# Performance work log

Hardware: AMD Instinct MI355X
Metric: run time of the kernel (lower is better)

Reference implementation:

```python
import jax, jax.numpy as jnp
import numpy as np

N, P, Q, T, J, B, H = 262144, 64, 64, 2048, 512, 8, 64


def setup_inputs() -> dict:
    key = jax.random.key(0)
    ks = jax.random.split(key, 11)
    sH = 1.0 / np.sqrt(H).astype(np.float32)
    return {
        "idx": jax.random.randint(ks[0], (B,), 0, J),
        "seg_ids": jnp.sort(jax.random.randint(ks[1], (N,), 0, T)),
        "K": jax.random.normal(ks[2], (N, P), jnp.float32) * 0.1,
        "V": jax.random.normal(ks[3], (N, Q), jnp.float32),
        "S": jax.random.normal(ks[4], (P, J), jnp.float32) * 0.1,
        "W_ih": jax.random.normal(ks[5], (3 * H, Q), jnp.float32) * sH,
        "W_hh": jax.random.normal(ks[6], (3 * H, H), jnp.float32) * sH,
        "b_ih": jax.random.normal(ks[7], (3 * H,), jnp.float32) * sH,
        "b_hh": jax.random.normal(ks[8], (3 * H,), jnp.float32) * sH,
        "w_out": jax.random.normal(ks[9], (1, H), jnp.float32) * sH,
        "b_out": jax.random.normal(ks[10], (1,), jnp.float32) * sH,
    }


def reference(idx, seg_ids, K, V, S, W_ih, W_hh, b_ih, b_hh, w_out, b_out):
    # W[:, b] = K @ S[:, idx[b]]  -> [N, B]
    w = K @ S[:, idx]
    # ragged per-segment softmax over the N axis (segments = date windows)
    m = jax.ops.segment_max(w, seg_ids, num_segments=T)          # [T, B]
    e = jnp.exp(w - m[seg_ids])                                  # [N, B]
    denom = jax.ops.segment_sum(e, seg_ids, num_segments=T)     # [T, B]
    alpha = e / denom[seg_ids]                                   # [N, B]
    # weighted aggregation of V rows per segment: M[t, b] = sum_u alpha_u * V_u
    M = jax.ops.segment_sum(alpha[:, :, None] * V[:, None, :],
                            seg_ids, num_segments=T)             # [T, B, Q]
    X = jnp.transpose(M, (1, 0, 2))                              # [B, T, Q]

    # PyTorch GRU (gate order r,z,n). Faithful to the original bug: GRU was
    # built without batch_first=True, so axis 0 (B) is time, axis 1 (T) is batch.
    def step(h, x_t):  # x_t: [T, Q], h: [T, H]
        gi = x_t @ W_ih.T + b_ih                                 # [T, 3H]
        gh = h @ W_hh.T + b_hh                                   # [T, 3H]
        i_r, i_z, i_n = jnp.split(gi, 3, axis=1)
        h_r, h_z, h_n = jnp.split(gh, 3, axis=1)
        r = jax.nn.sigmoid(i_r + h_r)
        z = jax.nn.sigmoid(i_z + h_z)
        n = jnp.tanh(i_n + r * h_n)
        h_new = (1.0 - z) * n + z * h
        return h_new, h_new

    h0 = jnp.zeros((T, H), X.dtype)
    _, hs = jax.lax.scan(step, h0, X)                            # [B, T, H]
    preds = hs @ w_out.T + b_out                                 # [B, T, 1]
    return preds
```

## Files before the change

### kernel.cpp

```cpp
#include <hip/hip_runtime.h>
#include <math.h>

#define NN 262144
#define PP 64
#define QQ 64
#define TT 2048
#define JJ 512
#define BB 8
#define HH 64

__device__ __forceinline__ float lane_bcast(float v, int l) {
  return __int_as_float(__builtin_amdgcn_readlane(__float_as_int(v), l));
}

__global__ void k_prep(const int* __restrict__ seg_ids, const int* __restrict__ idx,
                       const float* __restrict__ S, int* __restrict__ seg_start,
                       float* __restrict__ s_cols) {
  int tid = blockIdx.x * blockDim.x + threadIdx.x;
  if (tid <= TT) {
    int lo = 0, hi = NN;
    while (lo < hi) {
      int mid = (lo + hi) >> 1;
      int v = seg_ids[mid];
      if (v < tid) lo = mid + 1; else hi = mid;
    }
    seg_start[tid] = lo;
  }
  int t2 = tid - (TT + 1);
  if (t2 >= 0 && t2 < PP * BB) {
    int p = t2 >> 3, b = t2 & 7;
    s_cols[b * PP + p] = S[p * JJ + idx[b]];
  }
}

__global__ __launch_bounds__(256) void k_w(const float* __restrict__ Kmat,
                                           const float* __restrict__ s_cols,
                                           float* __restrict__ ew) {
  __shared__ __align__(16) float s_lds[BB * PP];
  int tid = threadIdx.x;
  for (int i = tid; i < BB * PP; i += 256) s_lds[i] = s_cols[i];
  __syncthreads();
  int n = blockIdx.x * 64 + (tid >> 2);
  int sub = tid & 3;
  const float4* Kp = reinterpret_cast<const float4*>(Kmat + (size_t)n * PP + sub * 16);
  float4 kq[4];
#pragma unroll
  for (int j = 0; j < 4; ++j) kq[j] = Kp[j];
  float acc[8];
#pragma unroll
  for (int b = 0; b < 8; ++b) acc[b] = 0.f;
#pragma unroll
  for (int j4 = 0; j4 < 4; ++j4) {
    float4 kk = kq[j4];
#pragma unroll
    for (int b = 0; b < 8; ++b) {
      const float4 sv = *reinterpret_cast<const float4*>(&s_lds[b * PP + sub * 16 + j4 * 4]);
      acc[b] += kk.x * sv.x + kk.y * sv.y + kk.z * sv.z + kk.w * sv.w;
    }
  }
#pragma unroll
  for (int b = 0; b < 8; ++b) {
    acc[b] += __shfl_xor(acc[b], 1);
    acc[b] += __shfl_xor(acc[b], 2);
  }
  float ox = (sub == 0) ? acc[0] : (sub == 1) ? acc[2] : (sub == 2) ? acc[4] : acc[6];
  float oy = (sub == 0) ? acc[1] : (sub == 1) ? acc[3] : (sub == 2) ? acc[5] : acc[7];
  reinterpret_cast<float2*>(ew + (size_t)n * 8)[sub] =
      make_float2(__expf(ox), __expf(oy));
}

#define PSTRIDE 520
__global__ __launch_bounds__(256) void k_segp(const float* __restrict__ ew,
                                              const float* __restrict__ V,
                                              const int* __restrict__ seg_start,
                                              float* __restrict__ P) {
  int lane = threadIdx.x & 63, j = threadIdx.x >> 6;
  int t = blockIdx.x;
  int s = seg_start[t], e = seg_start[t + 1];
  int len = e - s;
  int chunk = (len + 3) >> 2;
  int b0 = s + j * chunk;
  int b1 = b0 + chunk; if (b1 > e) b1 = e;
  int slen = (b1 > b0) ? (b1 - b0) : 0;
  int rsub = lane >> 4;
  int qg = lane & 15;

  float4 acc[8];
#pragma unroll
  for (int b = 0; b < 8; ++b) acc[b] = make_float4(0.f, 0.f, 0.f, 0.f);
  float4 selo = make_float4(0.f, 0.f, 0.f, 0.f);
  float4 sehi = make_float4(0.f, 0.f, 0.f, 0.f);

#define PROC(RR)                                                                                           \
  {                                                                                                        \
    int r_ = (RR);                                                                                         \
    const float4* ewp_ = reinterpret_cast<const float4*>(ew + (size_t)r_ * 8);                             \
    float4 elo = ewp_[0], ehi = ewp_[1];                                                                   \
    float4 vv = reinterpret_cast<const float4*>(V + (size_t)r_ * QQ)[qg];                                  \
    selo.x += elo.x; selo.y += elo.y; selo.z += elo.z; selo.w += elo.w;                                    \
    sehi.x += ehi.x; sehi.y += ehi.y; sehi.z += ehi.z; sehi.w += ehi.w;                                    \
    acc[0].x += elo.x * vv.x; acc[0].y += elo.x * vv.y; acc[0].z += elo.x * vv.z; acc[0].w += elo.x * vv.w; \
    acc[1].x += elo.y * vv.x; acc[1].y += elo.y * vv.y; acc[1].z += elo.y * vv.z; acc[1].w += elo.y * vv.w; \
    acc[2].x += elo.z * vv.x; acc[2].y += elo.z * vv.y; acc[2].z += elo.z * vv.z; acc[2].w += elo.z * vv.w; \
    acc[3].x += elo.w * vv.x; acc[3].y += elo.w * vv.y; acc[3].z += elo.w * vv.z; acc[3].w += elo.w * vv.w; \
    acc[4].x += ehi.x * vv.x; acc[4].y += ehi.x * vv.y; acc[4].z += ehi.x * vv.z; acc[4].w += ehi.x * vv.w; \
    acc[5].x += ehi.y * vv.x; acc[5].y += ehi.y * vv.y; acc[5].z += ehi.y * vv.z; acc[5].w += ehi.y * vv.w; \
    acc[6].x += ehi.z * vv.x; acc[6].y += ehi.z * vv.y; acc[6].z += ehi.z * vv.z; acc[6].w += ehi.z * vv.w; \
    acc[7].x += ehi.w * vv.x; acc[7].y += ehi.w * vv.y; acc[7].z += ehi.w * vv.z; acc[7].w += ehi.w * vv.w; \
  }

  int nfull = slen >> 2, tail = slen & 3;
  for (int i = 0; i < nfull; ++i) PROC(b0 + i * 4 + rsub);
  if (tail && rsub < tail) PROC(b0 + nfull * 4 + rsub);
#undef PROC

#pragma unroll
  for (int b = 0; b < 8; ++b) {
    acc[b].x += __shfl_xor(acc[b].x, 16); acc[b].y += __shfl_xor(acc[b].y, 16);
    acc[b].z += __shfl_xor(acc[b].z, 16); acc[b].w += __shfl_xor(acc[b].w, 16);
    acc[b].x += __shfl_xor(acc[b].x, 32); acc[b].y += __shfl_xor(acc[b].y, 32);
    acc[b].z += __shfl_xor(acc[b].z, 32); acc[b].w += __shfl_xor(acc[b].w, 32);
  }
  selo.x += __shfl_xor(selo.x, 16); selo.y += __shfl_xor(selo.y, 16);
  selo.z += __shfl_xor(selo.z, 16); selo.w += __shfl_xor(selo.w, 16);
  sehi.x += __shfl_xor(sehi.x, 16); sehi.y += __shfl_xor(sehi.y, 16);
  sehi.z += __shfl_xor(sehi.z, 16); sehi.w += __shfl_xor(sehi.w, 16);
  selo.x += __shfl_xor(selo.x, 32); selo.y += __shfl_xor(selo.y, 32);
  selo.z += __shfl_xor(selo.z, 32); selo.w += __shfl_xor(selo.w, 32);
  sehi.x += __shfl_xor(sehi.x, 32); sehi.y += __shfl_xor(sehi.y, 32);
  sehi.z += __shfl_xor(sehi.z, 32); sehi.w += __shfl_xor(sehi.w, 32);

  float* Pp = P + ((size_t)t * 4 + j) * PSTRIDE;
  if (rsub == 0) {
#pragma unroll
    for (int b = 0; b < 8; ++b)
      *reinterpret_cast<float4*>(Pp + b * 64 + qg * 4) = acc[b];
    if (qg == 0) {
      Pp[512] = selo.x; Pp[513] = selo.y; Pp[514] = selo.z; Pp[515] = selo.w;
      Pp[516] = sehi.x; Pp[517] = sehi.y; Pp[518] = sehi.z; Pp[519] = sehi.w;
    }
  }
}

__global__ __launch_bounds__(256) void k_red(const float* __restrict__ P,
                                             float* __restrict__ M) {
  __shared__ float se[32];
  int t = blockIdx.x, tid = threadIdx.x;
  if (tid < 32) se[tid] = P[((size_t)t * 4 + (tid >> 3)) * PSTRIDE + 512 + (tid & 7)];
  __syncthreads();
  int o = tid * 2;
  int b = o >> 6;
  float dd = se[b] + se[8 + b] + se[16 + b] + se[24 + b];
  float inv = (dd > 0.f) ? 1.f / dd : 0.f;
  float sx = 0.f, sy = 0.f;
#pragma unroll
  for (int j = 0; j < 4; ++j) {
    float2 p = *reinterpret_cast<const float2*>(P + ((size_t)t * 4 + j) * PSTRIDE + o);
    sx += p.x; sy += p.y;
  }
  *reinterpret_cast<float2*>(M + (size_t)t * 512 + o) = make_float2(sx * inv, sy * inv);
}

__global__ __launch_bounds__(256) void k_gi(const float* __restrict__ M,
                                            const float* __restrict__ W_ih,
                                            const float* __restrict__ b_ih,
                                            float* __restrict__ GI) {
  __shared__ float Wt[64 * 193];
  int tid = threadIdx.x;
  for (int i = tid; i < 192 * 64; i += 256) {
    int g = i >> 6, k = i & 63;
    Wt[k * 193 + g] = W_ih[i];
  }
  __syncthreads();
  int lane = tid & 63, wv = tid >> 6;
  int row0 = blockIdx.x * 32 + wv * 8;
  float x[8];
#pragma unroll
  for (int rr = 0; rr < 8; ++rr) {
    int rho = row0 + rr;
    int b = rho >> 11, t = rho & 2047;
    x[rr] = M[((size_t)t * 8 + b) * 64 + lane];
  }
  float bi0 = b_ih[lane], bi1 = b_ih[64 + lane], bi2 = b_ih[128 + lane];
  float a0[8], a1[8], a2[8];
#pragma unroll
  for (int rr = 0; rr < 8; ++rr) { a0[rr] = bi0; a1[rr] = bi1; a2[rr] = bi2; }
#pragma unroll
  for (int k = 0; k < 64; ++k) {
    float w0 = Wt[k * 193 + lane];
    float w1 = Wt[k * 193 + 64 + lane];
    float w2 = Wt[k * 193 + 128 + lane];
#pragma unroll
    for (int rr = 0; rr < 8; ++rr) {
      float xk = lane_bcast(x[rr], k);
      a0[rr] += w0 * xk; a1[rr] += w1 * xk; a2[rr] += w2 * xk;
    }
  }
#pragma unroll
  for (int rr = 0; rr < 8; ++rr) {
    size_t rho = (size_t)row0 + rr;
    GI[rho * 192 + lane]       = a0[rr];
    GI[rho * 192 + 64 + lane]  = a1[rr];
    GI[rho * 192 + 128 + lane] = a2[rr];
  }
}

__global__ __launch_bounds__(256) void k_gru(const float* __restrict__ GI,
                                             const float* __restrict__ W_hh,
                                             const float* __restrict__ b_hh,
                                             const float* __restrict__ w_out,
                                             const float* __restrict__ b_out,
                                             float* __restrict__ preds) {
  __shared__ float Wt[64 * 193];
  int tid = threadIdx.x;
  for (int i = tid; i < 192 * 64; i += 256) {
    int g = i >> 6, k = i & 63;
    Wt[k * 193 + g] = W_hh[i];
  }
  __syncthreads();
  int lane = tid & 63, wv = tid >> 6;
  int t = blockIdx.x * 4 + wv;
  float bh0 = b_hh[lane], bh1 = b_hh[64 + lane], bh2 = b_hh[128 + lane];
  float wo = w_out[lane];
  float bo = b_out[0];

  float gr[8], gz[8], gn[8];
#pragma unroll
  for (int b = 0; b < 8; ++b) {
    size_t base = ((size_t)b * TT + t) * 192;
    gr[b] = GI[base + lane];
    gz[b] = GI[base + 64 + lane];
    gn[b] = GI[base + 128 + lane];
  }

  float h;
  {
    float r = 1.f / (1.f + __expf(-(gr[0] + bh0)));
    float z = 1.f / (1.f + __expf(-(gz[0] + bh1)));
    float nv = tanhf(gn[0] + r * bh2);
    h = (1.f - z) * nv;
    float pv = h * wo;
#pragma unroll
    for (int off = 32; off; off >>= 1) pv += __shfl_xor(pv, off);
    if (lane == 0) preds[t] = pv + bo;
  }
#pragma unroll
  for (int b = 1; b < 8; ++b) {
    float ar = bh0, az = bh1, an = bh2;
#pragma unroll
    for (int k = 0; k < 64; ++k) {
      float hk = lane_bcast(h, k);
      float w0 = Wt[k * 193 + lane];
      float w1 = Wt[k * 193 + 64 + lane];
      float w2 = Wt[k * 193 + 128 + lane];
      ar += w0 * hk; az += w1 * hk; an += w2 * hk;
    }
    float r = 1.f / (1.f + __expf(-(gr[b] + ar)));
    float z = 1.f / (1.f + __expf(-(gz[b] + az)));
    float nv = tanhf(gn[b] + r * an);
    h = (1.f - z) * nv + z * h;
    float pv = h * wo;
#pragma unroll
    for (int off = 32; off; off >>= 1) pv += __shfl_xor(pv, off);
    if (lane == 0) preds[(size_t)b * TT + t] = pv + bo;
  }
}

extern "C" void kernel_launch(void* const* d_in, const int* in_sizes, int n_in,
                              void* d_out, int out_size, void* d_ws, size_t ws_size,
                              hipStream_t stream) {
  const int*   idx     = (const int*)d_in[0];
  const int*   seg_ids = (const int*)d_in[1];
  const float* Kmat    = (const float*)d_in[2];
  const float* V       = (const float*)d_in[3];
  const float* S       = (const float*)d_in[4];
  const float* W_ih    = (const float*)d_in[5];
  const float* W_hh    = (const float*)d_in[6];
  const float* b_ih    = (const float*)d_in[7];
  const float* b_hh    = (const float*)d_in[8];
  const float* w_out   = (const float*)d_in[9];
  const float* b_out   = (const float*)d_in[10];
  float* out = (float*)d_out;

  char* ws = (char*)d_ws;
  int*   seg_start = (int*)(ws + 0);
  float* s_cols    = (float*)(ws + 8448);
  float* ew        = (float*)(ws + 10496);
  float* M         = (float*)(ws + 8399104);
  float* GI        = (float*)(ws + 12593408);
  float* P         = (float*)(ws + 25176320);

  hipLaunchKernelGGL(k_prep, dim3(11), dim3(256), 0, stream, seg_ids, idx, S, seg_start, s_cols);
  hipLaunchKernelGGL(k_w, dim3(NN / 64), dim3(256), 0, stream, Kmat, s_cols, ew);
  hipLaunchKernelGGL(k_segp, dim3(TT), dim3(256), 0, stream, ew, V, seg_start, P);
  hipLaunchKernelGGL(k_red, dim3(TT), dim3(256), 0, stream, P, M);
  hipLaunchKernelGGL(k_gi, dim3(512), dim3(256), 0, stream, M, W_ih, b_ih, GI);
  hipLaunchKernelGGL(k_gru, dim3(512), dim3(256), 0, stream, GI, W_hh, b_hh, w_out, b_out, out);
}
```

Baseline: 81.51 us.

## Process two GRU sequences per wave with swizzled float4 W_hh in LDS

The GRU kernel now keeps W_hh in row-major LDS with an XOR swizzle and reads it as float4, replacing the padded transposed scalar layout. Each wave advances two independent batch rows (t0, t0+1) so every weight load from LDS feeds two hidden states, and the grid shrinks from 512 to 256 blocks. The aim is to halve LDS traffic per step and increase ILP. The cost is higher register pressure and fewer blocks for the GPU's compute units.

```diff
diff --git a/kernel.cpp b/kernel.cpp
--- a/kernel.cpp
+++ b/kernel.cpp
@@ -211,58 +211,84 @@
                                              const float* __restrict__ w_out,
                                              const float* __restrict__ b_out,
                                              float* __restrict__ preds) {
-  __shared__ float Wt[64 * 193];
+  __shared__ __align__(16) float Wl[192 * 64];
   int tid = threadIdx.x;
-  for (int i = tid; i < 192 * 64; i += 256) {
-    int g = i >> 6, k = i & 63;
-    Wt[k * 193 + g] = W_hh[i];
+  for (int i = tid; i < 192 * 16; i += 256) {
+    int g = i >> 4, c = i & 15;
+    *reinterpret_cast<float4*>(&Wl[g * 64 + ((c ^ (g & 15)) * 4)]) =
+        *reinterpret_cast<const float4*>(W_hh + g * 64 + c * 4);
   }
   __syncthreads();
   int lane = tid & 63, wv = tid >> 6;
-  int t = blockIdx.x * 4 + wv;
+  int t0 = blockIdx.x * 8 + wv * 2;
   float bh0 = b_hh[lane], bh1 = b_hh[64 + lane], bh2 = b_hh[128 + lane];
   float wo = w_out[lane];
   float bo = b_out[0];
 
-  float gr[8], gz[8], gn[8];
+  float gr0[8], gz0[8], gn0[8], gr1[8], gz1[8], gn1[8];
 #pragma unroll
   for (int b = 0; b < 8; ++b) {
-    size_t base = ((size_t)b * TT + t) * 192;
-    gr[b] = GI[base + lane];
-    gz[b] = GI[base + 64 + lane];
-    gn[b] = GI[base + 128 + lane];
-  }
-
-  float h;
+    size_t base0 = ((size_t)b * TT + t0) * 192;
+    gr0[b] = GI[base0 + lane];
+    gz0[b] = GI[base0 + 64 + lane];
+    gn0[b] = GI[base0 + 128 + lane];
+    size_t base1 = base0 + 192;
+    gr1[b] = GI[base1 + lane];
+    gz1[b] = GI[base1 + 64 + lane];
+    gn1[b] = GI[base1 + 128 + lane];
+  }
+
+  const int sw = (lane & 15);
+  float h0, h1;
   {
-    float r = 1.f / (1.f + __expf(-(gr[0] + bh0)));
-    float z = 1.f / (1.f + __expf(-(gz[0] + bh1)));
-    float nv = tanhf(gn[0] + r * bh2);
-    h = (1.f - z) * nv;
-    float pv = h * wo;
-#pragma unroll
-    for (int off = 32; off; off >>= 1) pv += __shfl_xor(pv, off);
-    if (lane == 0) preds[t] = pv + bo;
+    float r0 = 1.f / (1.f + __expf(-(gr0[0] + bh0)));
+    float z0 = 1.f / (1.f + __expf(-(gz0[0] + bh1)));
+    float n0 = tanhf(gn0[0] + r0 * bh2);
+    h0 = (1.f - z0) * n0;
+    float r1 = 1.f / (1.f + __expf(-(gr1[0] + bh0)));
+    float z1 = 1.f / (1.f + __expf(-(gz1[0] + bh1)));
+    float n1 = tanhf(gn1[0] + r1 * bh2);
+    h1 = (1.f - z1) * n1;
+    float pv0 = h0 * wo, pv1 = h1 * wo;
+#pragma unroll
+    for (int off = 32; off; off >>= 1) { pv0 += __shfl_xor(pv0, off); pv1 += __shfl_xor(pv1, off); }
+    if (lane == 0) { preds[t0] = pv0 + bo; preds[t0 + 1] = pv1 + bo; }
   }
 #pragma unroll
   for (int b = 1; b < 8; ++b) {
-    float ar = bh0, az = bh1, an = bh2;
-#pragma unroll
-    for (int k = 0; k < 64; ++k) {
-      float hk = lane_bcast(h, k);
-      float w0 = Wt[k * 193 + lane];
-      float w1 = Wt[k * 193 + 64 + lane];
-      float w2 = Wt[k * 193 + 128 + lane];
-      ar += w0 * hk; az += w1 * hk; an += w2 * hk;
-    }
-    float r = 1.f / (1.f + __expf(-(gr[b] + ar)));
-    float z = 1.f / (1.f + __expf(-(gz[b] + az)));
-    float nv = tanhf(gn[b] + r * an);
-    h = (1.f - z) * nv + z * h;
-    float pv = h * wo;
-#pragma unroll
-    for (int off = 32; off; off >>= 1) pv += __shfl_xor(pv, off);
-    if (lane == 0) preds[(size_t)b * TT + t] = pv + bo;
+    float ar0 = bh0, az0 = bh1, an0 = bh2;
+    float ar1 = bh0, az1 = bh1, an1 = bh2;
+#pragma unroll
+    for (int c = 0; c < 16; ++c) {
+      const float4 w0 = *reinterpret_cast<const float4*>(&Wl[lane * 64 + ((c ^ sw) * 4)]);
+      const float4 w1 = *reinterpret_cast<const float4*>(&Wl[(64 + lane) * 64 + ((c ^ sw) * 4)]);
+      const float4 w2 = *reinterpret_cast<const float4*>(&Wl[(128 + lane) * 64 + ((c ^ sw) * 4)]);
+      float a0 = lane_bcast(h0, c * 4 + 0), a1 = lane_bcast(h0, c * 4 + 1);
+      float a2 = lane_bcast(h0, c * 4 + 2), a3 = lane_bcast(h0, c * 4 + 3);
+      ar0 += w0.x * a0 + w0.y * a1 + w0.z * a2 + w0.w * a3;
+      az0 += w1.x * a0 + w1.y * a1 + w1.z * a2 + w1.w * a3;
+      an0 += w2.x * a0 + w2.y * a1 + w2.z * a2 + w2.w * a3;
+      float c0 = lane_bcast(h1, c * 4 + 0), c1 = lane_bcast(h1, c * 4 + 1);
+      float c2 = lane_bcast(h1, c * 4 + 2), c3 = lane_bcast(h1, c * 4 + 3);
+      ar1 += w0.x * c0 + w0.y * c1 + w0.z * c2 + w0.w * c3;
+      az1 += w1.x * c0 + w1.y * c1 + w1.z * c2 + w1.w * c3;
+      an1 += w2.x * c0 + w2.y * c1 + w2.z * c2 + w2.w * c3;
+    }
+    float r0 = 1.f / (1.f + __expf(-(gr0[b] + ar0)));
+    float z0 = 1.f / (1.f + __expf(-(gz0[b] + az0)));
+    float n0 = tanhf(gn0[b] + r0 * an0);
+    h0 = (1.f - z0) * n0 + z0 * h0;
+    float r1 = 1.f / (1.f + __expf(-(gr1[b] + ar1)));
+    float z1 = 1.f / (1.f + __expf(-(gz1[b] + az1)));
+    float n1 = tanhf(gn1[b] + r1 * an1);
+    h1 = (1.f - z1) * n1 + z1 * h1;
+    float pv0 = h0 * wo, pv1 = h1 * wo;
+#pragma unroll
+    for (int off = 32; off; off >>= 1) { pv0 += __shfl_xor(pv0, off); pv1 += __shfl_xor(pv1, off); }
+    if (lane == 0) {
+      preds[(size_t)b * TT + t0] = pv0 + bo;
+      preds[(size_t)b * TT + t0 + 1] = pv1 + bo;
+    }
   }
 }
 
@@ -295,5 +321,5 @@
   hipLaunchKernelGGL(k_segp, dim3(TT), dim3(256), 0, stream, ew, V, seg_start, P);
   hipLaunchKernelGGL(k_red, dim3(TT), dim3(256), 0, stream, P, M);
   hipLaunchKernelGGL(k_gi, dim3(512), dim3(256), 0, stream, M, W_ih, b_ih, GI);
-  hipLaunchKernelGGL(k_gru, dim3(512), dim3(256), 0, stream, GI, W_hh, b_hh, w_out, b_out, out);
-}
+  hipLaunchKernelGGL(k_gru, dim3(TT / 8), dim3(256), 0, stream, GI, W_hh, b_hh, w_out, b_out, out);
+}
```

Result: slower. 84.14 us (+3.2%).

## Fuse prep and segment reduction into neighbors, read GRU weights from global

Applied to the files above, without the earlier changes.

Removes the prep kernel by gathering the S columns inside k_w and running the segment-bound binary search inside the segment kernel. The per-segment partial sums now go through shared memory instead of a global P buffer, which removes the separate reduction kernel. Together this cuts two launches and a round trip of the partials through global memory. The GRU kernel drops its LDS transpose of W_hh and reads float4 rows from global/L1 with a 4-way readlane grouping, and the segment loop is unrolled by two. The risks are redundant S gathers in every k_w block and more global traffic in the GRU loop.

```diff
diff --git a/kernel.cpp b/kernel.cpp
--- a/kernel.cpp
+++ b/kernel.cpp
@@ -13,32 +13,16 @@
   return __int_as_float(__builtin_amdgcn_readlane(__float_as_int(v), l));
 }
 
-__global__ void k_prep(const int* __restrict__ seg_ids, const int* __restrict__ idx,
-                       const float* __restrict__ S, int* __restrict__ seg_start,
-                       float* __restrict__ s_cols) {
-  int tid = blockIdx.x * blockDim.x + threadIdx.x;
-  if (tid <= TT) {
-    int lo = 0, hi = NN;
-    while (lo < hi) {
-      int mid = (lo + hi) >> 1;
-      int v = seg_ids[mid];
-      if (v < tid) lo = mid + 1; else hi = mid;
-    }
-    seg_start[tid] = lo;
-  }
-  int t2 = tid - (TT + 1);
-  if (t2 >= 0 && t2 < PP * BB) {
-    int p = t2 >> 3, b = t2 & 7;
-    s_cols[b * PP + p] = S[p * JJ + idx[b]];
-  }
-}
-
 __global__ __launch_bounds__(256) void k_w(const float* __restrict__ Kmat,
-                                           const float* __restrict__ s_cols,
+                                           const int* __restrict__ idx,
+                                           const float* __restrict__ S,
                                            float* __restrict__ ew) {
   __shared__ __align__(16) float s_lds[BB * PP];
   int tid = threadIdx.x;
-  for (int i = tid; i < BB * PP; i += 256) s_lds[i] = s_cols[i];
+  for (int i = tid; i < BB * PP; i += 256) {
+    int p = i >> 3, b = i & 7;
+    s_lds[b * PP + p] = S[p * JJ + idx[b]];
+  }
   __syncthreads();
   int n = blockIdx.x * 64 + (tid >> 2);
   int sub = tid & 3;
@@ -69,14 +53,27 @@
       make_float2(__expf(ox), __expf(oy));
 }
 
-#define PSTRIDE 520
-__global__ __launch_bounds__(256) void k_segp(const float* __restrict__ ew,
+__global__ __launch_bounds__(256) void k_seg2(const float* __restrict__ ew,
                                               const float* __restrict__ V,
-                                              const int* __restrict__ seg_start,
-                                              float* __restrict__ P) {
-  int lane = threadIdx.x & 63, j = threadIdx.x >> 6;
+                                              const int* __restrict__ seg_ids,
+                                              float* __restrict__ M) {
+  __shared__ __align__(16) float accred[4][8][64];
+  __shared__ float reds[4][8];
+  __shared__ int bounds[2];
+  int tid = threadIdx.x;
   int t = blockIdx.x;
-  int s = seg_start[t], e = seg_start[t + 1];
+  if (tid < 2) {
+    int target = t + tid;
+    int lo = 0, hi = NN;
+    while (lo < hi) {
+      int mid = (lo + hi) >> 1;
+      if (seg_ids[mid] < target) lo = mid + 1; else hi = mid;
+    }
+    bounds[tid] = lo;
+  }
+  __syncthreads();
+  int s = bounds[0], e = bounds[1];
+  int lane = tid & 63, j = tid >> 6;
   int len = e - s;
   int chunk = (len + 3) >> 2;
   int b0 = s + j * chunk;
@@ -110,7 +107,12 @@
   }
 
   int nfull = slen >> 2, tail = slen & 3;
-  for (int i = 0; i < nfull; ++i) PROC(b0 + i * 4 + rsub);
+  int i = 0;
+  for (; i + 2 <= nfull; i += 2) {
+    PROC(b0 + i * 4 + rsub);
+    PROC(b0 + (i + 1) * 4 + rsub);
+  }
+  if (i < nfull) PROC(b0 + i * 4 + rsub);
   if (tail && rsub < tail) PROC(b0 + nfull * 4 + rsub);
 #undef PROC
 
@@ -130,35 +132,23 @@
   sehi.x += __shfl_xor(sehi.x, 32); sehi.y += __shfl_xor(sehi.y, 32);
   sehi.z += __shfl_xor(sehi.z, 32); sehi.w += __shfl_xor(sehi.w, 32);
 
-  float* Pp = P + ((size_t)t * 4 + j) * PSTRIDE;
   if (rsub == 0) {
 #pragma unroll
     for (int b = 0; b < 8; ++b)
-      *reinterpret_cast<float4*>(Pp + b * 64 + qg * 4) = acc[b];
+      *reinterpret_cast<float4*>(&accred[j][b][qg * 4]) = acc[b];
     if (qg == 0) {
-      Pp[512] = selo.x; Pp[513] = selo.y; Pp[514] = selo.z; Pp[515] = selo.w;
-      Pp[516] = sehi.x; Pp[517] = sehi.y; Pp[518] = sehi.z; Pp[519] = sehi.w;
-    }
-  }
-}
-
-__global__ __launch_bounds__(256) void k_red(const float* __restrict__ P,
-                                             float* __restrict__ M) {
-  __shared__ float se[32];
-  int t = blockIdx.x, tid = threadIdx.x;
-  if (tid < 32) se[tid] = P[((size_t)t * 4 + (tid >> 3)) * PSTRIDE + 512 + (tid & 7)];
-  __syncthreads();
-  int o = tid * 2;
-  int b = o >> 6;
-  float dd = se[b] + se[8 + b] + se[16 + b] + se[24 + b];
-  float inv = (dd > 0.f) ? 1.f / dd : 0.f;
-  float sx = 0.f, sy = 0.f;
-#pragma unroll
-  for (int j = 0; j < 4; ++j) {
-    float2 p = *reinterpret_cast<const float2*>(P + ((size_t)t * 4 + j) * PSTRIDE + o);
-    sx += p.x; sy += p.y;
-  }
-  *reinterpret_cast<float2*>(M + (size_t)t * 512 + o) = make_float2(sx * inv, sy * inv);
+      reds[j][0] = selo.x; reds[j][1] = selo.y; reds[j][2] = selo.z; reds[j][3] = selo.w;
+      reds[j][4] = sehi.x; reds[j][5] = sehi.y; reds[j][6] = sehi.z; reds[j][7] = sehi.w;
+    }
+  }
+  __syncthreads();
+  for (int o = tid; o < 512; o += 256) {
+    int b = o >> 6, q = o & 63;
+    float dd = reds[0][b] + reds[1][b] + reds[2][b] + reds[3][b];
+    float inv = (dd > 0.f) ? 1.f / dd : 0.f;
+    float sum = accred[0][b][q] + accred[1][b][q] + accred[2][b][q] + accred[3][b][q];
+    M[(size_t)t * 512 + o] = sum * inv;
+  }
 }
 
 __global__ __launch_bounds__(256) void k_gi(const float* __restrict__ M,
@@ -211,18 +201,14 @@
                                              const float* __restrict__ w_out,
                                              const float* __restrict__ b_out,
                                              float* __restrict__ preds) {
-  __shared__ float Wt[64 * 193];
-  int tid = threadIdx.x;
-  for (int i = tid; i < 192 * 64; i += 256) {
-    int g = i >> 6, k = i & 63;
-    Wt[k * 193 + g] = W_hh[i];
-  }
-  __syncthreads();
-  int lane = tid & 63, wv = tid >> 6;
+  int lane = threadIdx.x & 63, wv = threadIdx.x >> 6;
   int t = blockIdx.x * 4 + wv;
   float bh0 = b_hh[lane], bh1 = b_hh[64 + lane], bh2 = b_hh[128 + lane];
   float wo = w_out[lane];
   float bo = b_out[0];
+  const float4* w0p = reinterpret_cast<const float4*>(W_hh + (size_t)lane * 64);
+  const float4* w1p = reinterpret_cast<const float4*>(W_hh + (size_t)(64 + lane) * 64);
+  const float4* w2p = reinterpret_cast<const float4*>(W_hh + (size_t)(128 + lane) * 64);
 
   float gr[8], gz[8], gn[8];
 #pragma unroll
@@ -248,12 +234,13 @@
   for (int b = 1; b < 8; ++b) {
     float ar = bh0, az = bh1, an = bh2;
 #pragma unroll
-    for (int k = 0; k < 64; ++k) {
-      float hk = lane_bcast(h, k);
-      float w0 = Wt[k * 193 + lane];
-      float w1 = Wt[k * 193 + 64 + lane];
-      float w2 = Wt[k * 193 + 128 + lane];
-      ar += w0 * hk; az += w1 * hk; an += w2 * hk;
+    for (int c = 0; c < 16; ++c) {
+      float4 w0 = w0p[c], w1 = w1p[c], w2 = w2p[c];
+      float a0 = lane_bcast(h, c * 4 + 0), a1 = lane_bcast(h, c * 4 + 1);
+      float a2 = lane_bcast(h, c * 4 + 2), a3 = lane_bcast(h, c * 4 + 3);
+      ar += w0.x * a0 + w0.y * a1 + w0.z * a2 + w0.w * a3;
+      az += w1.x * a0 + w1.y * a1 + w1.z * a2 + w1.w * a3;
+      an += w2.x * a0 + w2.y * a1 + w2.z * a2 + w2.w * a3;
     }
     float r = 1.f / (1.f + __expf(-(gr[b] + ar)));
     float z = 1.f / (1.f + __expf(-(gz[b] + az)));
@@ -283,17 +270,12 @@
   float* out = (float*)d_out;
 
   char* ws = (char*)d_ws;
-  int*   seg_start = (int*)(ws + 0);
-  float* s_cols    = (float*)(ws + 8448);
-  float* ew        = (float*)(ws + 10496);
-  float* M         = (float*)(ws + 8399104);
-  float* GI        = (float*)(ws + 12593408);
-  float* P         = (float*)(ws + 25176320);
-
-  hipLaunchKernelGGL(k_prep, dim3(11), dim3(256), 0, stream, seg_ids, idx, S, seg_start, s_cols);
-  hipLaunchKernelGGL(k_w, dim3(NN / 64), dim3(256), 0, stream, Kmat, s_cols, ew);
-  hipLaunchKernelGGL(k_segp, dim3(TT), dim3(256), 0, stream, ew, V, seg_start, P);
-  hipLaunchKernelGGL(k_red, dim3(TT), dim3(256), 0, stream, P, M);
+  float* ew = (float*)(ws + 0);
+  float* M  = (float*)(ws + 8388608);
+  float* GI = (float*)(ws + 12582912);
+
+  hipLaunchKernelGGL(k_w, dim3(NN / 64), dim3(256), 0, stream, Kmat, idx, S, ew);
+  hipLaunchKernelGGL(k_seg2, dim3(TT), dim3(256), 0, stream, ew, V, seg_ids, M);
   hipLaunchKernelGGL(k_gi, dim3(512), dim3(256), 0, stream, M, W_ih, b_ih, GI);
   hipLaunchKernelGGL(k_gru, dim3(512), dim3(256), 0, stream, GI, W_hh, b_hh, w_out, b_out, out);
 }
```

Result: slower. 136.1 us (+67.0%).
